# Optimization experiments

Hardware: AMD Instinct MI355X
Metric: run time of the kernel (lower is better)

The kernel has to match this reference:

```python
import jax, jax.numpy as jnp
import numpy as np


def setup_inputs() -> dict:
    key0 = jax.random.key(0)
    kq, kk, kv = jax.random.split(key0, 3)
    B, H, L, S, D = 2, 8, 2048, 2048, 64
    query = jax.random.normal(kq, (B, H, L, D), dtype=jnp.float32)
    key = jax.random.normal(kk, (B, H, S, D), dtype=jnp.float32)
    value = jax.random.normal(kv, (B, H, S, D), dtype=jnp.float32)
    return {"query": query, "key": key, "value": value}


def reference(query, key, value):
    # Original computes matmul(q[b,h,l,1,d,1], k[b,h,1,s,1,d]) -> [B,H,L,S,D,D]
    # outer products, divides by sqrt(query.shape[-1]) AFTER unsqueeze (==1, no-op),
    # then sums dims (4,5). That is algebraically exactly rowsum(q)*rowsum(k).
    qsum = query.sum(axis=-1)                       # [B,H,L]
    ksum = key.sum(axis=-1)                         # [B,H,S]
    score = qsum[..., :, None] * ksum[..., None, :]  # [B,H,L,S]
    attn = jax.nn.softmax(score, axis=-1)            # softmax over S
    out = jnp.einsum('bhls,bhsd->bhld', attn, value)  # [B,H,L,D]
    return out
```

## Files before the change

### kernel.cpp

```cpp
#include <hip/hip_runtime.h>
#include <hip/hip_bf16.h>

#define BH 16
#define L 2048
#define S 2048
#define DD 64
#define BMB 32
#define NPITCH 68
#define LDSPAD 8
#define LDW (DD + LDSPAD)

typedef __attribute__((ext_vector_type(4))) float f32x4;
typedef __bf16 bf16x8 __attribute__((ext_vector_type(8)));

union FragU {
  bf16x8 f;
  __hip_bfloat162 h2[4];
};

__device__ inline __hip_bfloat162 exp2pack(float al2, float nsl2, float k0,
                                           float k1, float& d) {
  float e0 = __builtin_amdgcn_exp2f(fmaf(al2, k0, nsl2));
  float e1 = __builtin_amdgcn_exp2f(fmaf(al2, k1, nsl2));
  d += e0 + e1;
  return __float22bfloat162_rn(make_float2(e0, e1));
}

__global__ __launch_bounds__(256) void prep_kernel(
    const float* __restrict__ k, const float* __restrict__ v,
    float* __restrict__ ks, __hip_bfloat16* __restrict__ vt) {
  __shared__ __hip_bfloat16 tile[DD][LDW];
  int t = threadIdx.x;
  if (blockIdx.x < 2048) {
    int g = blockIdx.x * 256 + t;
    int row = g >> 4;
    int l16 = g & 15;
    float4 x = reinterpret_cast<const float4*>(k + (size_t)row * DD)[l16];
    float s = x.x + x.y + x.z + x.w;
    s += __shfl_xor(s, 1);
    s += __shfl_xor(s, 2);
    s += __shfl_xor(s, 4);
    s += __shfl_xor(s, 8);
    if (l16 == 0) ks[row] = s;
  } else {
    int bid = blockIdx.x - 2048;
    int s0 = (bid & 31) * 64;
    int bh = bid >> 5;
    int srow = t >> 4;
    int d4 = (t & 15) * 4;
#pragma unroll
    for (int kk = 0; kk < 4; ++kk) {
      int s = srow + kk * 16;
      float4 val = *reinterpret_cast<const float4*>(
          v + ((size_t)(bh * S + s0 + s)) * DD + d4);
      tile[d4 + 0][s] = __float2bfloat16(val.x);
      tile[d4 + 1][s] = __float2bfloat16(val.y);
      tile[d4 + 2][s] = __float2bfloat16(val.z);
      tile[d4 + 3][s] = __float2bfloat16(val.w);
    }
    __syncthreads();
    int dd = t >> 3;
    int j = t & 7;
#pragma unroll
    for (int kk = 0; kk < 2; ++kk) {
      int d = dd + kk * 32;
      uint4 val = *reinterpret_cast<const uint4*>(&tile[d][j * 8]);
      *reinterpret_cast<uint4*>(vt + ((size_t)(bh * DD + d)) * S + s0 + j * 8) =
          val;
    }
  }
}

__global__ __launch_bounds__(256, 4) void attn_kernel(
    const float* __restrict__ q, const __hip_bfloat16* __restrict__ vt,
    const float* __restrict__ ks, float* __restrict__ out) {
  int l0 = blockIdx.x * BMB;
  int bh = blockIdx.y;

  __shared__ float numLDS[4][BMB][NPITCH];
  __shared__ float dLDS[4][BMB];
  __shared__ float a_row[BMB];
  __shared__ float red[16];

  int t = threadIdx.x;
  int lane = t & 63;
  int w = t >> 6;
  int m = lane & 15;
  int qd = lane >> 4;

  const float* ksb = ks + (size_t)bh * S;
  const __hip_bfloat16* vtb = vt + (size_t)bh * DD * S;

  {
    int r = t >> 3;
    int p = t & 7;
    const float* qp = q + ((size_t)(bh * L + l0 + r)) * DD + p * 8;
    float4 x0 = reinterpret_cast<const float4*>(qp)[0];
    float4 x1 = reinterpret_cast<const float4*>(qp)[1];
    float s = (x0.x + x0.y + x0.z + x0.w) + (x1.x + x1.y + x1.z + x1.w);
    s += __shfl_xor(s, 1);
    s += __shfl_xor(s, 2);
    s += __shfl_xor(s, 4);
    if (p == 0) a_row[r] = s;
  }
  {
    const float* kp = ksb + t * 8;
    float4 y0 = reinterpret_cast<const float4*>(kp)[0];
    float4 y1 = reinterpret_cast<const float4*>(kp)[1];
    float mx = fmaxf(fmaxf(fmaxf(y0.x, y0.y), fmaxf(y0.z, y0.w)),
                     fmaxf(fmaxf(y1.x, y1.y), fmaxf(y1.z, y1.w)));
    float mn = fminf(fminf(fminf(y0.x, y0.y), fminf(y0.z, y0.w)),
                     fminf(fminf(y1.x, y1.y), fminf(y1.z, y1.w)));
#pragma unroll
    for (int off = 1; off < 64; off <<= 1) {
      mx = fmaxf(mx, __shfl_xor(mx, off));
      mn = fminf(mn, __shfl_xor(mn, off));
    }
    if (lane == 0) {
      red[w] = mx;
      red[8 + w] = mn;
    }
  }
  __syncthreads();

  float kmax = fmaxf(fmaxf(red[0], red[1]), fmaxf(red[2], red[3]));
  float kmin = fminf(fminf(red[8], red[9]), fminf(red[10], red[11]));
  const float LOG2E = 1.44269504088896f;
  float ar0 = a_row[m];
  float ar1 = a_row[16 + m];
  float al20 = ar0 * LOG2E, al21 = ar1 * LOG2E;
  float nsl20 = -al20 * ((ar0 > 0.f) ? kmax : kmin);
  float nsl21 = -al21 * ((ar1 > 0.f) ? kmax : kmin);

  f32x4 acc[2][4];
#pragma unroll
  for (int a = 0; a < 2; ++a)
#pragma unroll
    for (int c = 0; c < 4; ++c) acc[a][c] = (f32x4){0.f, 0.f, 0.f, 0.f};
  float ds0a = 0.f, ds0b = 0.f, ds1a = 0.f, ds1b = 0.f;

  const __hip_bfloat16* bp0 = vtb + (size_t)(0 * 16 + m) * S + qd * 8;
  const __hip_bfloat16* bp1 = vtb + (size_t)(1 * 16 + m) * S + qd * 8;
  const __hip_bfloat16* bp2 = vtb + (size_t)(2 * 16 + m) * S + qd * 8;
  const __hip_bfloat16* bp3 = vtb + (size_t)(3 * 16 + m) * S + qd * 8;

  int sw = w * (S / 4);
  for (int it = 0; it < (S / 4) / 64; ++it) {
    int sb = sw + it * 64;
    float4 kA0 = *reinterpret_cast<const float4*>(ksb + sb + qd * 8);
    float4 kA1 = *reinterpret_cast<const float4*>(ksb + sb + qd * 8 + 4);
    float4 kB0 = *reinterpret_cast<const float4*>(ksb + sb + 32 + qd * 8);
    float4 kB1 = *reinterpret_cast<const float4*>(ksb + sb + 32 + qd * 8 + 4);
    uint4 b00 = *reinterpret_cast<const uint4*>(bp0 + sb);
    uint4 b01 = *reinterpret_cast<const uint4*>(bp1 + sb);
    uint4 b02 = *reinterpret_cast<const uint4*>(bp2 + sb);
    uint4 b03 = *reinterpret_cast<const uint4*>(bp3 + sb);
    uint4 b10 = *reinterpret_cast<const uint4*>(bp0 + sb + 32);
    uint4 b11 = *reinterpret_cast<const uint4*>(bp1 + sb + 32);
    uint4 b12 = *reinterpret_cast<const uint4*>(bp2 + sb + 32);
    uint4 b13 = *reinterpret_cast<const uint4*>(bp3 + sb + 32);

    FragU e00, e01, e10, e11;
    e00.h2[0] = exp2pack(al20, nsl20, kA0.x, kA0.y, ds0a);
    e00.h2[1] = exp2pack(al20, nsl20, kA0.z, kA0.w, ds0a);
    e00.h2[2] = exp2pack(al20, nsl20, kA1.x, kA1.y, ds0a);
    e00.h2[3] = exp2pack(al20, nsl20, kA1.z, kA1.w, ds0a);
    e01.h2[0] = exp2pack(al20, nsl20, kB0.x, kB0.y, ds0b);
    e01.h2[1] = exp2pack(al20, nsl20, kB0.z, kB0.w, ds0b);
    e01.h2[2] = exp2pack(al20, nsl20, kB1.x, kB1.y, ds0b);
    e01.h2[3] = exp2pack(al20, nsl20, kB1.z, kB1.w, ds0b);
    e10.h2[0] = exp2pack(al21, nsl21, kA0.x, kA0.y, ds1a);
    e10.h2[1] = exp2pack(al21, nsl21, kA0.z, kA0.w, ds1a);
    e10.h2[2] = exp2pack(al21, nsl21, kA1.x, kA1.y, ds1a);
    e10.h2[3] = exp2pack(al21, nsl21, kA1.z, kA1.w, ds1a);
    e11.h2[0] = exp2pack(al21, nsl21, kB0.x, kB0.y, ds1b);
    e11.h2[1] = exp2pack(al21, nsl21, kB0.z, kB0.w, ds1b);
    e11.h2[2] = exp2pack(al21, nsl21, kB1.x, kB1.y, ds1b);
    e11.h2[3] = exp2pack(al21, nsl21, kB1.z, kB1.w, ds1b);

    acc[0][0] = __builtin_amdgcn_mfma_f32_16x16x32_bf16(
        e00.f, __builtin_bit_cast(bf16x8, b00), acc[0][0], 0, 0, 0);
    acc[0][1] = __builtin_amdgcn_mfma_f32_16x16x32_bf16(
        e00.f, __builtin_bit_cast(bf16x8, b01), acc[0][1], 0, 0, 0);
    acc[0][2] = __builtin_amdgcn_mfma_f32_16x16x32_bf16(
        e00.f, __builtin_bit_cast(bf16x8, b02), acc[0][2], 0, 0, 0);
    acc[0][3] = __builtin_amdgcn_mfma_f32_16x16x32_bf16(
        e00.f, __builtin_bit_cast(bf16x8, b03), acc[0][3], 0, 0, 0);
    acc[1][0] = __builtin_amdgcn_mfma_f32_16x16x32_bf16(
        e10.f, __builtin_bit_cast(bf16x8, b00), acc[1][0], 0, 0, 0);
    acc[1][1] = __builtin_amdgcn_mfma_f32_16x16x32_bf16(
        e10.f, __builtin_bit_cast(bf16x8, b01), acc[1][1], 0, 0, 0);
    acc[1][2] = __builtin_amdgcn_mfma_f32_16x16x32_bf16(
        e10.f, __builtin_bit_cast(bf16x8, b02), acc[1][2], 0, 0, 0);
    acc[1][3] = __builtin_amdgcn_mfma_f32_16x16x32_bf16(
        e10.f, __builtin_bit_cast(bf16x8, b03), acc[1][3], 0, 0, 0);
    acc[0][0] = __builtin_amdgcn_mfma_f32_16x16x32_bf16(
        e01.f, __builtin_bit_cast(bf16x8, b10), acc[0][0], 0, 0, 0);
    acc[0][1] = __builtin_amdgcn_mfma_f32_16x16x32_bf16(
        e01.f, __builtin_bit_cast(bf16x8, b11), acc[0][1], 0, 0, 0);
    acc[0][2] = __builtin_amdgcn_mfma_f32_16x16x32_bf16(
        e01.f, __builtin_bit_cast(bf16x8, b12), acc[0][2], 0, 0, 0);
    acc[0][3] = __builtin_amdgcn_mfma_f32_16x16x32_bf16(
        e01.f, __builtin_bit_cast(bf16x8, b13), acc[0][3], 0, 0, 0);
    acc[1][0] = __builtin_amdgcn_mfma_f32_16x16x32_bf16(
        e11.f, __builtin_bit_cast(bf16x8, b10), acc[1][0], 0, 0, 0);
    acc[1][1] = __builtin_amdgcn_mfma_f32_16x16x32_bf16(
        e11.f, __builtin_bit_cast(bf16x8, b11), acc[1][1], 0, 0, 0);
    acc[1][2] = __builtin_amdgcn_mfma_f32_16x16x32_bf16(
        e11.f, __builtin_bit_cast(bf16x8, b12), acc[1][2], 0, 0, 0);
    acc[1][3] = __builtin_amdgcn_mfma_f32_16x16x32_bf16(
        e11.f, __builtin_bit_cast(bf16x8, b13), acc[1][3], 0, 0, 0);
  }

  float ds0 = ds0a + ds0b;
  float ds1 = ds1a + ds1b;
  ds0 += __shfl_xor(ds0, 16);
  ds0 += __shfl_xor(ds0, 32);
  ds1 += __shfl_xor(ds1, 16);
  ds1 += __shfl_xor(ds1, 32);
  if (qd == 0) {
    dLDS[w][m] = ds0;
    dLDS[w][16 + m] = ds1;
  }
#pragma unroll
  for (int a = 0; a < 2; ++a)
#pragma unroll
    for (int c = 0; c < 4; ++c)
#pragma unroll
      for (int i = 0; i < 4; ++i)
        numLDS[w][a * 16 + qd * 4 + i][c * 16 + m] = acc[a][c][i];
  __syncthreads();

  {
    int r = t >> 3;
    int cg = (t & 7) * 8;
    float4 n0 = *reinterpret_cast<const float4*>(&numLDS[0][r][cg]);
    float4 n1 = *reinterpret_cast<const float4*>(&numLDS[0][r][cg + 4]);
#pragma unroll
    for (int ww = 1; ww < 4; ++ww) {
      float4 p0 = *reinterpret_cast<const float4*>(&numLDS[ww][r][cg]);
      float4 p1 = *reinterpret_cast<const float4*>(&numLDS[ww][r][cg + 4]);
      n0.x += p0.x; n0.y += p0.y; n0.z += p0.z; n0.w += p0.w;
      n1.x += p1.x; n1.y += p1.y; n1.z += p1.z; n1.w += p1.w;
    }
    float inv = 1.0f / (dLDS[0][r] + dLDS[1][r] + dLDS[2][r] + dLDS[3][r]);
    n0.x *= inv; n0.y *= inv; n0.z *= inv; n0.w *= inv;
    n1.x *= inv; n1.y *= inv; n1.z *= inv; n1.w *= inv;
    float* ob = out + ((size_t)(bh * L + l0 + r)) * DD + cg;
    reinterpret_cast<float4*>(ob)[0] = n0;
    reinterpret_cast<float4*>(ob)[1] = n1;
  }
}

extern "C" void kernel_launch(void* const* d_in, const int* in_sizes, int n_in,
                              void* d_out, int out_size, void* d_ws,
                              size_t ws_size, hipStream_t stream) {
  const float* q = (const float*)d_in[0];
  const float* k = (const float*)d_in[1];
  const float* v = (const float*)d_in[2];
  float* out = (float*)d_out;
  float* ws = (float*)d_ws;

  float* ks = ws;
  __hip_bfloat16* vt = (__hip_bfloat16*)(ws + BH * S);

  prep_kernel<<<2048 + 512, 256, 0, stream>>>(k, v, ks, vt);
  attn_kernel<<<dim3(L / BMB, BH), 256, 0, stream>>>(q, vt, ks, out);
}
```

Before: 110.9 us.

## Tile transposed V into contiguous 64x64 blocks and swizzle block-to-head mapping

The prep kernel now stores transposed bf16 V as contiguous per-(head, 64-key) tiles of 64x64 instead of one strided row per feature, so each MFMA B-fragment load reads from a compact 8KB tile. The attention launch becomes 1D, with a swizzle that interleaves heads so that concurrently running blocks (likely spread across XCDs) work on different heads, aiming for better L2 locality. The inner loop is restructured to 32 keys per iteration with unroll 2. This lowers per-iteration register use, but the loop body becomes less explicitly interleaved.

```diff
diff --git a/kernel.cpp b/kernel.cpp
--- a/kernel.cpp
+++ b/kernel.cpp
@@ -44,8 +44,9 @@
     if (l16 == 0) ks[row] = s;
   } else {
     int bid = blockIdx.x - 2048;
-    int s0 = (bid & 31) * 64;
-    int bh = bid >> 5;
+    int bh = (bid & 7) * 2 + ((bid >> 3) & 1);
+    int st = bid >> 4;
+    int s0 = st * 64;
     int srow = t >> 4;
     int d4 = (t & 15) * 4;
 #pragma unroll
@@ -59,14 +60,14 @@
       tile[d4 + 3][s] = __float2bfloat16(val.w);
     }
     __syncthreads();
+    __hip_bfloat16* tb = vt + ((size_t)(bh * 32 + st)) * (DD * 64);
     int dd = t >> 3;
     int j = t & 7;
 #pragma unroll
     for (int kk = 0; kk < 2; ++kk) {
       int d = dd + kk * 32;
       uint4 val = *reinterpret_cast<const uint4*>(&tile[d][j * 8]);
-      *reinterpret_cast<uint4*>(vt + ((size_t)(bh * DD + d)) * S + s0 + j * 8) =
-          val;
+      *reinterpret_cast<uint4*>(tb + d * 64 + j * 8) = val;
     }
   }
 }
@@ -74,8 +75,9 @@
 __global__ __launch_bounds__(256, 4) void attn_kernel(
     const float* __restrict__ q, const __hip_bfloat16* __restrict__ vt,
     const float* __restrict__ ks, float* __restrict__ out) {
-  int l0 = blockIdx.x * BMB;
-  int bh = blockIdx.y;
+  int lin = blockIdx.x;
+  int bh = (lin & 7) * 2 + ((lin >> 3) & 1);
+  int l0 = (lin >> 4) * BMB;
 
   __shared__ float numLDS[4][BMB][NPITCH];
   __shared__ float dLDS[4][BMB];
@@ -89,7 +91,7 @@
   int qd = lane >> 4;
 
   const float* ksb = ks + (size_t)bh * S;
-  const __hip_bfloat16* vtb = vt + (size_t)bh * DD * S;
+  const __hip_bfloat16* tb = vt + ((size_t)bh * 32) * (DD * 64);
 
   {
     int r = t >> 3;
@@ -137,83 +139,49 @@
   for (int a = 0; a < 2; ++a)
 #pragma unroll
     for (int c = 0; c < 4; ++c) acc[a][c] = (f32x4){0.f, 0.f, 0.f, 0.f};
-  float ds0a = 0.f, ds0b = 0.f, ds1a = 0.f, ds1b = 0.f;
-
-  const __hip_bfloat16* bp0 = vtb + (size_t)(0 * 16 + m) * S + qd * 8;
-  const __hip_bfloat16* bp1 = vtb + (size_t)(1 * 16 + m) * S + qd * 8;
-  const __hip_bfloat16* bp2 = vtb + (size_t)(2 * 16 + m) * S + qd * 8;
-  const __hip_bfloat16* bp3 = vtb + (size_t)(3 * 16 + m) * S + qd * 8;
+  float ds0 = 0.f, ds1 = 0.f;
 
   int sw = w * (S / 4);
-  for (int it = 0; it < (S / 4) / 64; ++it) {
-    int sb = sw + it * 64;
-    float4 kA0 = *reinterpret_cast<const float4*>(ksb + sb + qd * 8);
-    float4 kA1 = *reinterpret_cast<const float4*>(ksb + sb + qd * 8 + 4);
-    float4 kB0 = *reinterpret_cast<const float4*>(ksb + sb + 32 + qd * 8);
-    float4 kB1 = *reinterpret_cast<const float4*>(ksb + sb + 32 + qd * 8 + 4);
-    uint4 b00 = *reinterpret_cast<const uint4*>(bp0 + sb);
-    uint4 b01 = *reinterpret_cast<const uint4*>(bp1 + sb);
-    uint4 b02 = *reinterpret_cast<const uint4*>(bp2 + sb);
-    uint4 b03 = *reinterpret_cast<const uint4*>(bp3 + sb);
-    uint4 b10 = *reinterpret_cast<const uint4*>(bp0 + sb + 32);
-    uint4 b11 = *reinterpret_cast<const uint4*>(bp1 + sb + 32);
-    uint4 b12 = *reinterpret_cast<const uint4*>(bp2 + sb + 32);
-    uint4 b13 = *reinterpret_cast<const uint4*>(bp3 + sb + 32);
-
-    FragU e00, e01, e10, e11;
-    e00.h2[0] = exp2pack(al20, nsl20, kA0.x, kA0.y, ds0a);
-    e00.h2[1] = exp2pack(al20, nsl20, kA0.z, kA0.w, ds0a);
-    e00.h2[2] = exp2pack(al20, nsl20, kA1.x, kA1.y, ds0a);
-    e00.h2[3] = exp2pack(al20, nsl20, kA1.z, kA1.w, ds0a);
-    e01.h2[0] = exp2pack(al20, nsl20, kB0.x, kB0.y, ds0b);
-    e01.h2[1] = exp2pack(al20, nsl20, kB0.z, kB0.w, ds0b);
-    e01.h2[2] = exp2pack(al20, nsl20, kB1.x, kB1.y, ds0b);
-    e01.h2[3] = exp2pack(al20, nsl20, kB1.z, kB1.w, ds0b);
-    e10.h2[0] = exp2pack(al21, nsl21, kA0.x, kA0.y, ds1a);
-    e10.h2[1] = exp2pack(al21, nsl21, kA0.z, kA0.w, ds1a);
-    e10.h2[2] = exp2pack(al21, nsl21, kA1.x, kA1.y, ds1a);
-    e10.h2[3] = exp2pack(al21, nsl21, kA1.z, kA1.w, ds1a);
-    e11.h2[0] = exp2pack(al21, nsl21, kB0.x, kB0.y, ds1b);
-    e11.h2[1] = exp2pack(al21, nsl21, kB0.z, kB0.w, ds1b);
-    e11.h2[2] = exp2pack(al21, nsl21, kB1.x, kB1.y, ds1b);
-    e11.h2[3] = exp2pack(al21, nsl21, kB1.z, kB1.w, ds1b);
+#pragma unroll 2
+  for (int kt = 0; kt < (S / 4) / 32; ++kt) {
+    int sb = sw + kt * 32;
+    const __hip_bfloat16* tp =
+        tb + (size_t)(sb >> 6) * (DD * 64) + (sb & 63) + qd * 8;
+    uint4 b0 = *reinterpret_cast<const uint4*>(tp + (0 * 16 + m) * 64);
+    uint4 b1 = *reinterpret_cast<const uint4*>(tp + (1 * 16 + m) * 64);
+    uint4 b2 = *reinterpret_cast<const uint4*>(tp + (2 * 16 + m) * 64);
+    uint4 b3 = *reinterpret_cast<const uint4*>(tp + (3 * 16 + m) * 64);
+    float4 kv0 = *reinterpret_cast<const float4*>(ksb + sb + qd * 8);
+    float4 kv1 = *reinterpret_cast<const float4*>(ksb + sb + qd * 8 + 4);
+
+    FragU e0, e1;
+    e0.h2[0] = exp2pack(al20, nsl20, kv0.x, kv0.y, ds0);
+    e0.h2[1] = exp2pack(al20, nsl20, kv0.z, kv0.w, ds0);
+    e0.h2[2] = exp2pack(al20, nsl20, kv1.x, kv1.y, ds0);
+    e0.h2[3] = exp2pack(al20, nsl20, kv1.z, kv1.w, ds0);
+    e1.h2[0] = exp2pack(al21, nsl21, kv0.x, kv0.y, ds1);
+    e1.h2[1] = exp2pack(al21, nsl21, kv0.z, kv0.w, ds1);
+    e1.h2[2] = exp2pack(al21, nsl21, kv1.x, kv1.y, ds1);
+    e1.h2[3] = exp2pack(al21, nsl21, kv1.z, kv1.w, ds1);
 
     acc[0][0] = __builtin_amdgcn_mfma_f32_16x16x32_bf16(
-        e00.f, __builtin_bit_cast(bf16x8, b00), acc[0][0], 0, 0, 0);
+        e0.f, __builtin_bit_cast(bf16x8, b0), acc[0][0], 0, 0, 0);
     acc[0][1] = __builtin_amdgcn_mfma_f32_16x16x32_bf16(
-        e00.f, __builtin_bit_cast(bf16x8, b01), acc[0][1], 0, 0, 0);
+        e0.f, __builtin_bit_cast(bf16x8, b1), acc[0][1], 0, 0, 0);
     acc[0][2] = __builtin_amdgcn_mfma_f32_16x16x32_bf16(
-        e00.f, __builtin_bit_cast(bf16x8, b02), acc[0][2], 0, 0, 0);
+        e0.f, __builtin_bit_cast(bf16x8, b2), acc[0][2], 0, 0, 0);
     acc[0][3] = __builtin_amdgcn_mfma_f32_16x16x32_bf16(
-        e00.f, __builtin_bit_cast(bf16x8, b03), acc[0][3], 0, 0, 0);
+        e0.f, __builtin_bit_cast(bf16x8, b3), acc[0][3], 0, 0, 0);
     acc[1][0] = __builtin_amdgcn_mfma_f32_16x16x32_bf16(
-        e10.f, __builtin_bit_cast(bf16x8, b00), acc[1][0], 0, 0, 0);
+        e1.f, __builtin_bit_cast(bf16x8, b0), acc[1][0], 0, 0, 0);
     acc[1][1] = __builtin_amdgcn_mfma_f32_16x16x32_bf16(
-        e10.f, __builtin_bit_cast(bf16x8, b01), acc[1][1], 0, 0, 0);
+        e1.f, __builtin_bit_cast(bf16x8, b1), acc[1][1], 0, 0, 0);
     acc[1][2] = __builtin_amdgcn_mfma_f32_16x16x32_bf16(
-        e10.f, __builtin_bit_cast(bf16x8, b02), acc[1][2], 0, 0, 0);
+        e1.f, __builtin_bit_cast(bf16x8, b2), acc[1][2], 0, 0, 0);
     acc[1][3] = __builtin_amdgcn_mfma_f32_16x16x32_bf16(
-        e10.f, __builtin_bit_cast(bf16x8, b03), acc[1][3], 0, 0, 0);
-    acc[0][0] = __builtin_amdgcn_mfma_f32_16x16x32_bf16(
-        e01.f, __builtin_bit_cast(bf16x8, b10), acc[0][0], 0, 0, 0);
-    acc[0][1] = __builtin_amdgcn_mfma_f32_16x16x32_bf16(
-        e01.f, __builtin_bit_cast(bf16x8, b11), acc[0][1], 0, 0, 0);
-    acc[0][2] = __builtin_amdgcn_mfma_f32_16x16x32_bf16(
-        e01.f, __builtin_bit_cast(bf16x8, b12), acc[0][2], 0, 0, 0);
-    acc[0][3] = __builtin_amdgcn_mfma_f32_16x16x32_bf16(
-        e01.f, __builtin_bit_cast(bf16x8, b13), acc[0][3], 0, 0, 0);
-    acc[1][0] = __builtin_amdgcn_mfma_f32_16x16x32_bf16(
-        e11.f, __builtin_bit_cast(bf16x8, b10), acc[1][0], 0, 0, 0);
-    acc[1][1] = __builtin_amdgcn_mfma_f32_16x16x32_bf16(
-        e11.f, __builtin_bit_cast(bf16x8, b11), acc[1][1], 0, 0, 0);
-    acc[1][2] = __builtin_amdgcn_mfma_f32_16x16x32_bf16(
-        e11.f, __builtin_bit_cast(bf16x8, b12), acc[1][2], 0, 0, 0);
-    acc[1][3] = __builtin_amdgcn_mfma_f32_16x16x32_bf16(
-        e11.f, __builtin_bit_cast(bf16x8, b13), acc[1][3], 0, 0, 0);
-  }
-
-  float ds0 = ds0a + ds0b;
-  float ds1 = ds1a + ds1b;
+        e1.f, __builtin_bit_cast(bf16x8, b3), acc[1][3], 0, 0, 0);
+  }
+
   ds0 += __shfl_xor(ds0, 16);
   ds0 += __shfl_xor(ds0, 32);
   ds1 += __shfl_xor(ds1, 16);
@@ -265,5 +233,5 @@
   __hip_bfloat16* vt = (__hip_bfloat16*)(ws + BH * S);
 
   prep_kernel<<<2048 + 512, 256, 0, stream>>>(k, v, ks, vt);
-  attn_kernel<<<dim3(L / BMB, BH), 256, 0, stream>>>(q, vt, ks, out);
-}
+  attn_kernel<<<(L / BMB) * BH, 256, 0, stream>>>(q, vt, ks, out);
+}
```

Result: slower. 113.8 us (+2.6%).
